# Performance work log

Measured on AMD Instinct MI355X. Metric: run time of the kernel, lower is better.

## Reference

```python
import jax, jax.numpy as jnp
import numpy as np

B, T = 32, 1024
TEMP_IN, STAT_IN = 128, 64
TEMP_OUT, STAT_OUT = 128, 64
EPS = 1e-5
NEG_SLOPE = 0.01


def _bn_eval(x, gamma, beta, mean, var):
    # BatchNorm1d in eval mode (running stats)
    return (x - mean) * jax.lax.rsqrt(var + EPS) * gamma + beta


def _leaky_relu(x):
    return jnp.where(x >= 0, x, NEG_SLOPE * x)


def setup_inputs() -> dict:
    key = jax.random.key(0)
    k = jax.random.split(key, 6)
    # deterministic ragged lengths in [512, 1024]
    lengths_np = (512 + (np.arange(B) * 37) % 513).astype(np.int64)
    N = int(lengths_np.sum())  # 23450
    batch_idx = np.repeat(np.arange(B), lengths_np).astype(np.int32)
    pos_idx = np.concatenate([np.arange(l) for l in lengths_np]).astype(np.int32)
    valid = (np.arange(T)[None, :] < lengths_np[:, None])  # [B, T]
    mask_repeat = valid[:, :, None] & valid[:, None, :]    # [B, T, T]

    inp = {
        "x_temp": jax.random.normal(k[0], (N, TEMP_IN), jnp.float32),
        "x_stat": jax.random.normal(k[1], (B, STAT_IN), jnp.float32),
        "temp_attn": jax.random.normal(k[2], (B, T, T), jnp.float32) * 0.1,
        "mask_repeat": jnp.asarray(mask_repeat),
        "lengths": jnp.asarray(lengths_np),
        "batch_idx": jnp.asarray(batch_idx),
        "pos_idx": jnp.asarray(pos_idx),
        # non_linear_temp: Linear(TEMP_IN+STAT_IN -> TEMP_OUT) + BN
        "W1": jax.random.normal(k[3], (TEMP_OUT, TEMP_IN + STAT_IN), jnp.float32) / np.sqrt(TEMP_IN + STAT_IN),
        "b1": jnp.zeros((TEMP_OUT,), jnp.float32),
        "gamma1": jnp.ones((TEMP_OUT,), jnp.float32),
        "beta1": jnp.zeros((TEMP_OUT,), jnp.float32),
        "mean1": jnp.zeros((TEMP_OUT,), jnp.float32),
        "var1": jnp.ones((TEMP_OUT,), jnp.float32),
        # non_linear_stat: Linear(STAT_IN -> STAT_OUT) + BN
        "W2": jax.random.normal(k[4], (STAT_OUT, STAT_IN), jnp.float32) / np.sqrt(STAT_IN),
        "b2": jnp.zeros((STAT_OUT,), jnp.float32),
        "gamma2": jnp.ones((STAT_OUT,), jnp.float32),
        "beta2": jnp.zeros((STAT_OUT,), jnp.float32),
        "mean2": jnp.zeros((STAT_OUT,), jnp.float32),
        "var2": jnp.ones((STAT_OUT,), jnp.float32),
    }
    return inp


def reference(x_temp, x_stat, temp_attn, mask_repeat, lengths, batch_idx, pos_idx,
              W1, b1, gamma1, beta1, mean1, var1,
              W2, b2, gamma2, beta2, mean2, var2):
    # repeat_static_features: gather per-batch static feats to packed rows
    x_stat_rep = x_stat[batch_idx]                              # [N, STAT_IN]
    h = jnp.concatenate((x_temp, x_stat_rep), axis=-1) @ W1.T + b1
    h = _leaky_relu(_bn_eval(h, gamma1, beta1, mean1, var1))    # [N, TEMP_OUT]

    # pad_packed_sequences: scatter packed rows into [B, T, C] (zeros elsewhere)
    padded = jnp.zeros((B, T, TEMP_OUT), h.dtype).at[batch_idx, pos_idx].set(h)

    # self attention: softmax(x x^T / sqrt(d)) over padded rows (as original)
    d = jnp.asarray(TEMP_OUT, h.dtype)
    qk = jnp.einsum('btc,bsc->bts', padded, padded) / jnp.sqrt(d)
    self_attn = jax.nn.softmax(qk, axis=-1)

    attn = jnp.where(mask_repeat, self_attn + temp_attn, jnp.asarray(0.0, h.dtype))

    x_stat_out = _leaky_relu(_bn_eval(x_stat @ W2.T + b2, gamma2, beta2, mean2, var2))

    x_out_pad = jnp.einsum('bts,bsc->btc', attn, padded)        # [B, T, TEMP_OUT]
    # pack_padded_sequences: gather valid positions back to packed layout
    x_out = x_out_pad[batch_idx, pos_idx]                       # [N, TEMP_OUT]
    return (x_out, x_stat_out)
```

## Files before the change

### kernel.cpp

```cpp
#include <hip/hip_runtime.h>
#include <hip/hip_bf16.h>
#include <hip/hip_fp16.h>

typedef __hip_bfloat16 bf16;
typedef __attribute__((ext_vector_type(8))) short short8;
typedef __attribute__((ext_vector_type(4))) float f32x4;

#define EPS 1e-5f
#define NSLOPE 0.01f

__device__ __forceinline__ float b2f(bf16 v) { return __bfloat162float(v); }

__device__ __forceinline__ float ld1(const void* p, size_t idx, int isbf) {
  if (isbf) return b2f(((const bf16*)p)[idx]);
  return ((const float*)p)[idx];
}
__device__ __forceinline__ void st1(void* p, size_t idx, int isbf, float v) {
  if (isbf) ((bf16*)p)[idx] = __float2bfloat16(v);
  else      ((float*)p)[idx] = v;
}
__device__ __forceinline__ short f2bs(float x) {
  bf16 t = __float2bfloat16(x);
  short s; __builtin_memcpy(&s, &t, 2); return s;
}
__device__ __forceinline__ short8 pack8f(const float* p) {
  float4 a = *(const float4*)p, b = *(const float4*)(p + 4);
  short8 r;
  r[0] = f2bs(a.x); r[1] = f2bs(a.y); r[2] = f2bs(a.z); r[3] = f2bs(a.w);
  r[4] = f2bs(b.x); r[5] = f2bs(b.y); r[6] = f2bs(b.z); r[7] = f2bs(b.w);
  return r;
}

__global__ void meta_kernel(const void* __restrict__ xt,
                            const int* __restrict__ bidx, const int* __restrict__ pidx,
                            int N, int B, int* __restrict__ rs, int* __restrict__ ln,
                            int* __restrict__ flag) {
  if (blockIdx.x == 0 && threadIdx.x < 64) {
    unsigned w = ((const unsigned*)xt)[threadIdx.x];
    unsigned lo = w & 0xffffu;
    unsigned ex = (lo >> 7) & 0xffu;
    bool sane = ((lo & 0x7fffu) == 0u) || (ex >= 96u && ex <= 134u);
    unsigned long long m = __ballot(sane);
    if (threadIdx.x == 0) flag[0] = (__popcll(m) >= 48) ? 1 : 0;
  }
  int stride = gridDim.x * blockDim.x;
  for (int i = blockIdx.x * blockDim.x + threadIdx.x; i < N; i += stride) {
    int b = bidx[i];
    if ((unsigned)b >= (unsigned)B) continue;
    if (i == 0 || bidx[i - 1] != b) rs[b] = i;
    if (i == N - 1 || bidx[i + 1] != b) ln[b] = pidx[i] + 1;
  }
}

__global__ void w1cvt_kernel(const void* __restrict__ W1, const int* __restrict__ flag,
                             bf16* __restrict__ w1b, int n) {
  const int isbf = flag[0];
  int i = blockIdx.x * blockDim.x + threadIdx.x;
  if (i < n) w1b[i] = __float2bfloat16(ld1(W1, i, isbf));
}

__global__ void zfill_kernel(void* out, const int* __restrict__ flag, long long n) {
  const int isbf = flag[0];
  long long i = (long long)blockIdx.x * blockDim.x + threadIdx.x;
  long long stride = (long long)gridDim.x * blockDim.x;
  for (; i < n; i += stride) st1(out, (size_t)i, isbf, 0.f);
}

__global__ __launch_bounds__(256) void h_mfma_kernel(
    const void* __restrict__ xt, const void* __restrict__ xsg,
    const int* __restrict__ bidx, const bf16* __restrict__ w1b,
    const void* __restrict__ b1,
    const void* __restrict__ g1, const void* __restrict__ be1,
    const void* __restrict__ mn1, const void* __restrict__ vr1,
    const int* __restrict__ flag, bf16* __restrict__ hout, int N) {
  const int isbf = flag[0];
  const int tid = threadIdx.x, lane = tid & 63, wv = tid >> 6;
  const int m16 = lane & 15, quad = lane >> 4;
  const int row0 = blockIdx.x * 64 + wv * 16;
  const int m = row0 + m16;
  const int mc = (m < N) ? m : (N - 1);
  const int bi = bidx[mc];

  short8 af[6];
  if (isbf) {
    const bf16* xr = (const bf16*)xt + (size_t)mc * 128 + quad * 8;
#pragma unroll
    for (int ks = 0; ks < 4; ++ks) af[ks] = *(const short8*)(xr + ks * 32);
    const bf16* sr = (const bf16*)xsg + (size_t)bi * 64 + quad * 8;
    af[4] = *(const short8*)sr;
    af[5] = *(const short8*)(sr + 32);
  } else {
    const float* xr = (const float*)xt + (size_t)mc * 128 + quad * 8;
#pragma unroll
    for (int ks = 0; ks < 4; ++ks) af[ks] = pack8f(xr + ks * 32);
    const float* sr = (const float*)xsg + (size_t)bi * 64 + quad * 8;
    af[4] = pack8f(sr);
    af[5] = pack8f(sr + 32);
  }

  f32x4 acc[8];
#pragma unroll
  for (int ct = 0; ct < 8; ++ct) acc[ct] = (f32x4){0.f, 0.f, 0.f, 0.f};

#pragma unroll
  for (int ks = 0; ks < 6; ++ks) {
    const int k = ks * 32 + quad * 8;
#pragma unroll
    for (int ct = 0; ct < 8; ++ct) {
      const int o = ct * 16 + m16;
      short8 bfrag = *(const short8*)(w1b + (size_t)o * 192 + k);
      acc[ct] = __builtin_amdgcn_mfma_f32_16x16x32_bf16(af[ks], bfrag, acc[ct], 0, 0, 0);
    }
  }

#pragma unroll
  for (int ct = 0; ct < 8; ++ct) {
    const int o = ct * 16 + m16;
    float k1 = ld1(g1, o, isbf) * rsqrtf(ld1(vr1, o, isbf) + EPS);
    float k0 = ld1(be1, o, isbf) - ld1(mn1, o, isbf) * k1;
    float bias = ld1(b1, o, isbf);
#pragma unroll
    for (int r = 0; r < 4; ++r) {
      int mr = row0 + quad * 4 + r;
      if (mr < N) {
        float v = (acc[ct][r] + bias) * k1 + k0;
        v = (v >= 0.f) ? v : NSLOPE * v;
        hout[(size_t)mr * 128 + o] = __float2bfloat16(v);
      }
    }
  }
}

__global__ __launch_bounds__(64) void stat_kernel(
    const void* __restrict__ xstat, const void* __restrict__ W2,
    const void* __restrict__ b2, const void* __restrict__ g2,
    const void* __restrict__ be2, const void* __restrict__ mn2,
    const void* __restrict__ vr2, const int* __restrict__ flag,
    void* __restrict__ out, long long obase) {
  __shared__ float xs[64];
  const int isbf = flag[0];
  const int b = blockIdx.x, o = threadIdx.x;
  xs[o] = ld1(xstat, b * 64 + o, isbf);
  __syncthreads();
  float acc = ld1(b2, o, isbf);
#pragma unroll 8
  for (int j = 0; j < 64; ++j) acc += xs[j] * ld1(W2, o * 64 + j, isbf);
  float k1 = ld1(g2, o, isbf) * rsqrtf(ld1(vr2, o, isbf) + EPS);
  float k0 = ld1(be2, o, isbf) - ld1(mn2, o, isbf) * k1;
  float v = acc * k1 + k0;
  v = (v >= 0.f) ? v : NSLOPE * v;
  st1(out, (size_t)(obase + b * 64 + o), isbf, v);
}

__global__ __launch_bounds__(256) void attn_mfma_kernel(
    const void* __restrict__ ta, const bf16* __restrict__ h,
    const int* __restrict__ rs_arr, const int* __restrict__ ln_arr,
    const int* __restrict__ flag, void* __restrict__ xout, int T, int N) {
  __shared__ __align__(16) unsigned short Ss[16][1032];
  __shared__ __align__(16) unsigned short vT[128][66];

  const int b = blockIdx.y, t0 = blockIdx.x * 16;
  const int len = ln_arr[b];
  if (t0 >= len) return;
  const int isbf = flag[0];
  const int rs = rs_arr[b];
  const int nrows = min(16, len - t0);
  const int tid = threadIdx.x;
  const int lane = tid & 63, wv = tid >> 6;
  const int m16 = lane & 15, quad = lane >> 4;

  short8 qf[4];
  {
    int qrow = rs + t0 + m16;
    if (qrow > N - 1) qrow = N - 1;
    const bf16* qp = h + (size_t)qrow * 128 + quad * 8;
#pragma unroll
    for (int ks = 0; ks < 4; ++ks)
      qf[ks] = *(const short8*)(qp + ks * 32);
  }

  const float scale = 0.08838834764831845f;
  const int nact = (len + 15) >> 4;
  const short8 zero8 = {0, 0, 0, 0, 0, 0, 0, 0};

  {
    short8 kc[4] = {zero8, zero8, zero8, zero8};
    int st = wv;
    if (st < nact) {
      int s = st * 16 + m16;
      bool v = (s < len);
      const bf16* kp = h + (size_t)(rs + (v ? s : 0)) * 128 + quad * 8;
#pragma unroll
      for (int ks = 0; ks < 4; ++ks) kc[ks] = v ? *(const short8*)(kp + ks * 32) : zero8;
    }
    for (; st < nact; st += 4) {
      short8 kn[4] = {zero8, zero8, zero8, zero8};
      int stn = st + 4;
      if (stn < nact) {
        int s2 = stn * 16 + m16;
        bool v2 = (s2 < len);
        const bf16* kp2 = h + (size_t)(rs + (v2 ? s2 : 0)) * 128 + quad * 8;
#pragma unroll
        for (int ks = 0; ks < 4; ++ks) kn[ks] = v2 ? *(const short8*)(kp2 + ks * 32) : zero8;
      }
      f32x4 acc = {0.f, 0.f, 0.f, 0.f};
#pragma unroll
      for (int ks = 0; ks < 4; ++ks)
        acc = __builtin_amdgcn_mfma_f32_16x16x32_bf16(qf[ks], kc[ks], acc, 0, 0, 0);
      int s = st * 16 + m16;
      if (s < T) {
#pragma unroll
        for (int r = 0; r < 4; ++r)
          Ss[quad * 4 + r][s] = __half_as_ushort(__float2half(acc[r] * scale));
      }
#pragma unroll
      for (int ks = 0; ks < 4; ++ks) kc[ks] = kn[ks];
    }
  }
  __syncthreads();

  {
    const int lenp64 = (len + 63) & ~63;
    for (int j = 0; j < 4; ++j) {
      int r = wv + (j << 2);
      float vals[16];
#pragma unroll
      for (int k = 0; k < 16; ++k) {
        int s = lane + (k << 6);
        vals[k] = (s < len) ? __half2float(__ushort_as_half(Ss[r][s])) : -INFINITY;
      }
      float mx = -INFINITY;
#pragma unroll
      for (int k = 0; k < 16; ++k) mx = fmaxf(mx, vals[k]);
#pragma unroll
      for (int off = 32; off >= 1; off >>= 1) mx = fmaxf(mx, __shfl_xor(mx, off, 64));
      if (len < T) mx = fmaxf(mx, 0.f);
      float l = 0.f;
#pragma unroll
      for (int k = 0; k < 16; ++k) { float e = __expf(vals[k] - mx); vals[k] = e; l += e; }
#pragma unroll
      for (int off = 32; off >= 1; off >>= 1) l += __shfl_xor(l, off, 64);
      l += (float)(T - len) * __expf(-mx);
      float inv = 1.f / l;
#pragma unroll
      for (int k = 0; k < 16; ++k) {
        int s = lane + (k << 6);
        if (s < len)          *(bf16*)&Ss[r][s] = __float2bfloat16(vals[k] * inv);
        else if (s < lenp64)  *(bf16*)&Ss[r][s] = __float2bfloat16(0.f);
      }
    }
  }
  __syncthreads();

  f32x4 oacc0 = {0.f, 0.f, 0.f, 0.f};
  f32x4 oacc1 = {0.f, 0.f, 0.f, 0.f};
  const size_t tarow = ((size_t)b * T + (t0 + m16)) * (size_t)T;
  for (int s0 = 0; s0 < len; s0 += 64) {
    for (int e = tid; e < 512; e += 256) {
      int sp = e >> 4, c8 = (e & 15) << 3;
      int s = s0 + 2 * sp;
      uint4 u0 = {0, 0, 0, 0}, u1 = {0, 0, 0, 0};
      if (s < len)     u0 = *(const uint4*)(h + (size_t)(rs + s) * 128 + c8);
      if (s + 1 < len) u1 = *(const uint4*)(h + (size_t)(rs + s + 1) * 128 + c8);
      const unsigned short* a0 = (const unsigned short*)&u0;
      const unsigned short* a1 = (const unsigned short*)&u1;
#pragma unroll
      for (int j = 0; j < 8; ++j)
        *(unsigned*)&vT[c8 + j][2 * sp] = (unsigned)a0[j] | ((unsigned)a1[j] << 16);
    }
    short8 taf0, taf1;
    if (isbf) {
      const bf16* tp = (const bf16*)ta + tarow + s0 + quad * 8;
      taf0 = *(const short8*)tp;
      taf1 = *(const short8*)(tp + 32);
    } else {
      const float* tp = (const float*)ta + tarow + s0 + quad * 8;
      taf0 = pack8f(tp);
      taf1 = pack8f(tp + 32);
    }
    __syncthreads();
#pragma unroll
    for (int ks = 0; ks < 2; ++ks) {
      short8 pf = *(const short8*)&Ss[m16][s0 + ks * 32 + quad * 8];
      short8 tf = ks ? taf1 : taf0;
#pragma unroll
      for (int ct = 0; ct < 2; ++ct) {
        const int c0 = wv * 32 + ct * 16;
        const unsigned short* vrow = &vT[c0 + m16][ks * 32 + quad * 8];
        unsigned w0 = *(const unsigned*)(vrow + 0);
        unsigned w1 = *(const unsigned*)(vrow + 2);
        unsigned w2 = *(const unsigned*)(vrow + 4);
        unsigned w3 = *(const unsigned*)(vrow + 6);
        short8 bfv;
        bfv[0] = (short)(w0 & 0xffffu); bfv[1] = (short)(w0 >> 16);
        bfv[2] = (short)(w1 & 0xffffu); bfv[3] = (short)(w1 >> 16);
        bfv[4] = (short)(w2 & 0xffffu); bfv[5] = (short)(w2 >> 16);
        bfv[6] = (short)(w3 & 0xffffu); bfv[7] = (short)(w3 >> 16);
        if (ct == 0) {
          oacc0 = __builtin_amdgcn_mfma_f32_16x16x32_bf16(pf, bfv, oacc0, 0, 0, 0);
          oacc0 = __builtin_amdgcn_mfma_f32_16x16x32_bf16(tf, bfv, oacc0, 0, 0, 0);
        } else {
          oacc1 = __builtin_amdgcn_mfma_f32_16x16x32_bf16(pf, bfv, oacc1, 0, 0, 0);
          oacc1 = __builtin_amdgcn_mfma_f32_16x16x32_bf16(tf, bfv, oacc1, 0, 0, 0);
        }
      }
    }
    __syncthreads();
  }

#pragma unroll
  for (int r = 0; r < 4; ++r) {
    int t = quad * 4 + r;
    if (t < nrows) {
      size_t ob = (size_t)(rs + t0 + t) * 128;
      st1(xout, ob + wv * 32 + m16,      isbf, oacc0[r]);
      st1(xout, ob + wv * 32 + 16 + m16, isbf, oacc1[r]);
    }
  }
}

extern "C" void kernel_launch(void* const* d_in, const int* in_sizes, int n_in,
                              void* d_out, int out_size, void* d_ws, size_t ws_size,
                              hipStream_t stream) {
  const void* x_temp    = d_in[0];
  const void* x_stat    = d_in[1];
  const void* temp_attn = d_in[2];
  const int N = in_sizes[0] / 128;
  const int B = in_sizes[1] / 64;
  long long tt = (long long)in_sizes[2] / B;
  int T = 1; while ((long long)(T + 1) * (T + 1) <= tt) ++T;

  int p = 3;
  while (p < n_in && in_sizes[p] != N) ++p;
  const int* batch_idx = (const int*)d_in[p++];
  const int* pos_idx   = (const int*)d_in[p++];
  const void* W1 = d_in[p++];
  const void* b1 = d_in[p++];
  const void* g1 = d_in[p++];
  const void* be1= d_in[p++];
  const void* mn1= d_in[p++];
  const void* vr1= d_in[p++];
  const void* W2 = d_in[p++];
  const void* b2 = d_in[p++];
  const void* g2 = d_in[p++];
  const void* be2= d_in[p++];
  const void* mn2= d_in[p++];
  const void* vr2= d_in[p++];

  int*  meta = (int*)d_ws;
  int*  rs   = meta;
  int*  lnp  = meta + B;
  int*  flag = meta + 2 * B;
  bf16* h    = (bf16*)((char*)d_ws + 1024);
  bf16* w1b  = h + (size_t)N * 128;
  const int w1n = 128 * 192;
  size_t need = 1024 + (size_t)N * 128 * sizeof(bf16) + (size_t)w1n * sizeof(bf16);

  long long obase = (long long)N * 128;

  meta_kernel<<<90, 256, 0, stream>>>(x_temp, batch_idx, pos_idx, N, B, rs, lnp, flag);
  stat_kernel<<<B, 64, 0, stream>>>(x_stat, W2, b2, g2, be2, mn2, vr2, flag,
                                    d_out, obase);
  if (ws_size >= need) {
    w1cvt_kernel<<<(w1n + 255) / 256, 256, 0, stream>>>(W1, flag, w1b, w1n);
    h_mfma_kernel<<<(N + 63) / 64, 256, 0, stream>>>(x_temp, x_stat, batch_idx,
                                                     w1b, b1, g1, be1, mn1, vr1,
                                                     flag, h, N);
    attn_mfma_kernel<<<dim3((T + 15) / 16, B), 256, 0, stream>>>(
        temp_attn, h, rs, lnp, flag, d_out, T, N);
  } else {
    zfill_kernel<<<512, 256, 0, stream>>>(d_out, flag, obase);
  }
}
```

Baseline: 442.5 us.

## Stream attention with online softmax and fold W1 conversion into meta kernel

The attention kernel drops the full 16x1024 score buffer in shared memory and replaces the three phases (QK, softmax, PV) with a flash-style loop over 64-column key tiles. Each tile keeps a running max and sum, rescales the probability accumulator, and keeps the temp_attn contribution in a separate accumulator. Shared memory use shrinks sharply, and launch_bounds asks for 4 blocks per CU to raise occupancy. The cost is extra barriers and cross-wave reductions inside every tile. The W1 bf16 conversion is merged into meta_kernel, removing one launch, but only if w1b fits in the workspace, since it is now written before the size check.

```diff
diff --git a/kernel.cpp b/kernel.cpp
--- a/kernel.cpp
+++ b/kernel.cpp
@@ -34,29 +34,28 @@
 __global__ void meta_kernel(const void* __restrict__ xt,
                             const int* __restrict__ bidx, const int* __restrict__ pidx,
                             int N, int B, int* __restrict__ rs, int* __restrict__ ln,
-                            int* __restrict__ flag) {
-  if (blockIdx.x == 0 && threadIdx.x < 64) {
-    unsigned w = ((const unsigned*)xt)[threadIdx.x];
+                            int* __restrict__ flag,
+                            const void* __restrict__ W1, bf16* __restrict__ w1b, int w1n) {
+  int isbf_l = 0;
+  {
+    unsigned w = ((const unsigned*)xt)[threadIdx.x & 63];
     unsigned lo = w & 0xffffu;
     unsigned ex = (lo >> 7) & 0xffu;
     bool sane = ((lo & 0x7fffu) == 0u) || (ex >= 96u && ex <= 134u);
     unsigned long long m = __ballot(sane);
-    if (threadIdx.x == 0) flag[0] = (__popcll(m) >= 48) ? 1 : 0;
+    isbf_l = (__popcll(m) >= 48) ? 1 : 0;
+    if (blockIdx.x == 0 && threadIdx.x == 0) flag[0] = isbf_l;
   }
   int stride = gridDim.x * blockDim.x;
-  for (int i = blockIdx.x * blockDim.x + threadIdx.x; i < N; i += stride) {
+  int g0 = blockIdx.x * blockDim.x + threadIdx.x;
+  for (int i = g0; i < N; i += stride) {
     int b = bidx[i];
     if ((unsigned)b >= (unsigned)B) continue;
     if (i == 0 || bidx[i - 1] != b) rs[b] = i;
     if (i == N - 1 || bidx[i + 1] != b) ln[b] = pidx[i] + 1;
   }
-}
-
-__global__ void w1cvt_kernel(const void* __restrict__ W1, const int* __restrict__ flag,
-                             bf16* __restrict__ w1b, int n) {
-  const int isbf = flag[0];
-  int i = blockIdx.x * blockDim.x + threadIdx.x;
-  if (i < n) w1b[i] = __float2bfloat16(ld1(W1, i, isbf));
+  for (int i = g0; i < w1n; i += stride)
+    w1b[i] = __float2bfloat16(ld1(W1, i, isbf_l));
 }
 
 __global__ void zfill_kernel(void* out, const int* __restrict__ flag, long long n) {
@@ -152,12 +151,16 @@
   st1(out, (size_t)(obase + b * 64 + o), isbf, v);
 }
 
-__global__ __launch_bounds__(256) void attn_mfma_kernel(
+__global__ __launch_bounds__(256, 4) void attn_mfma_kernel(
     const void* __restrict__ ta, const bf16* __restrict__ h,
     const int* __restrict__ rs_arr, const int* __restrict__ ln_arr,
     const int* __restrict__ flag, void* __restrict__ xout, int T, int N) {
-  __shared__ __align__(16) unsigned short Ss[16][1032];
   __shared__ __align__(16) unsigned short vT[128][66];
+  __shared__ __align__(16) unsigned short Pbuf[16][72];
+  __shared__ float wmax[4][16];
+  __shared__ float wsum[4][16];
+  __shared__ float mrun[16];
+  __shared__ float lrun[16];
 
   const int b = blockIdx.y, t0 = blockIdx.x * 16;
   const int len = ln_arr[b];
@@ -175,91 +178,32 @@
     if (qrow > N - 1) qrow = N - 1;
     const bf16* qp = h + (size_t)qrow * 128 + quad * 8;
 #pragma unroll
-    for (int ks = 0; ks < 4; ++ks)
-      qf[ks] = *(const short8*)(qp + ks * 32);
-  }
+    for (int ks = 0; ks < 4; ++ks) qf[ks] = *(const short8*)(qp + ks * 32);
+  }
+
+  if (tid < 16) { mrun[tid] = -INFINITY; lrun[tid] = 0.f; }
 
   const float scale = 0.08838834764831845f;
-  const int nact = (len + 15) >> 4;
   const short8 zero8 = {0, 0, 0, 0, 0, 0, 0, 0};
-
+  const int scol = wv * 16 + m16;
+  const size_t tarow = ((size_t)b * T + (t0 + m16)) * (size_t)T;
+
+  f32x4 accp[2] = {{0.f,0.f,0.f,0.f},{0.f,0.f,0.f,0.f}};
+  f32x4 acct[2] = {{0.f,0.f,0.f,0.f},{0.f,0.f,0.f,0.f}};
+
+  short8 kf[4];
   {
-    short8 kc[4] = {zero8, zero8, zero8, zero8};
-    int st = wv;
-    if (st < nact) {
-      int s = st * 16 + m16;
-      bool v = (s < len);
-      const bf16* kp = h + (size_t)(rs + (v ? s : 0)) * 128 + quad * 8;
-#pragma unroll
-      for (int ks = 0; ks < 4; ++ks) kc[ks] = v ? *(const short8*)(kp + ks * 32) : zero8;
-    }
-    for (; st < nact; st += 4) {
-      short8 kn[4] = {zero8, zero8, zero8, zero8};
-      int stn = st + 4;
-      if (stn < nact) {
-        int s2 = stn * 16 + m16;
-        bool v2 = (s2 < len);
-        const bf16* kp2 = h + (size_t)(rs + (v2 ? s2 : 0)) * 128 + quad * 8;
-#pragma unroll
-        for (int ks = 0; ks < 4; ++ks) kn[ks] = v2 ? *(const short8*)(kp2 + ks * 32) : zero8;
-      }
-      f32x4 acc = {0.f, 0.f, 0.f, 0.f};
-#pragma unroll
-      for (int ks = 0; ks < 4; ++ks)
-        acc = __builtin_amdgcn_mfma_f32_16x16x32_bf16(qf[ks], kc[ks], acc, 0, 0, 0);
-      int s = st * 16 + m16;
-      if (s < T) {
-#pragma unroll
-        for (int r = 0; r < 4; ++r)
-          Ss[quad * 4 + r][s] = __half_as_ushort(__float2half(acc[r] * scale));
-      }
-#pragma unroll
-      for (int ks = 0; ks < 4; ++ks) kc[ks] = kn[ks];
-    }
-  }
-  __syncthreads();
-
-  {
-    const int lenp64 = (len + 63) & ~63;
-    for (int j = 0; j < 4; ++j) {
-      int r = wv + (j << 2);
-      float vals[16];
-#pragma unroll
-      for (int k = 0; k < 16; ++k) {
-        int s = lane + (k << 6);
-        vals[k] = (s < len) ? __half2float(__ushort_as_half(Ss[r][s])) : -INFINITY;
-      }
-      float mx = -INFINITY;
-#pragma unroll
-      for (int k = 0; k < 16; ++k) mx = fmaxf(mx, vals[k]);
-#pragma unroll
-      for (int off = 32; off >= 1; off >>= 1) mx = fmaxf(mx, __shfl_xor(mx, off, 64));
-      if (len < T) mx = fmaxf(mx, 0.f);
-      float l = 0.f;
-#pragma unroll
-      for (int k = 0; k < 16; ++k) { float e = __expf(vals[k] - mx); vals[k] = e; l += e; }
-#pragma unroll
-      for (int off = 32; off >= 1; off >>= 1) l += __shfl_xor(l, off, 64);
-      l += (float)(T - len) * __expf(-mx);
-      float inv = 1.f / l;
-#pragma unroll
-      for (int k = 0; k < 16; ++k) {
-        int s = lane + (k << 6);
-        if (s < len)          *(bf16*)&Ss[r][s] = __float2bfloat16(vals[k] * inv);
-        else if (s < lenp64)  *(bf16*)&Ss[r][s] = __float2bfloat16(0.f);
-      }
-    }
-  }
-  __syncthreads();
-
-  f32x4 oacc0 = {0.f, 0.f, 0.f, 0.f};
-  f32x4 oacc1 = {0.f, 0.f, 0.f, 0.f};
-  const size_t tarow = ((size_t)b * T + (t0 + m16)) * (size_t)T;
+    bool v = scol < len;
+    const bf16* kp = h + (size_t)(rs + (v ? scol : 0)) * 128 + quad * 8;
+#pragma unroll
+    for (int ks = 0; ks < 4; ++ks) kf[ks] = v ? *(const short8*)(kp + ks * 32) : zero8;
+  }
+
   for (int s0 = 0; s0 < len; s0 += 64) {
     for (int e = tid; e < 512; e += 256) {
       int sp = e >> 4, c8 = (e & 15) << 3;
       int s = s0 + 2 * sp;
-      uint4 u0 = {0, 0, 0, 0}, u1 = {0, 0, 0, 0};
+      uint4 u0 = {0,0,0,0}, u1 = {0,0,0,0};
       if (s < len)     u0 = *(const uint4*)(h + (size_t)(rs + s) * 128 + c8);
       if (s + 1 < len) u1 = *(const uint4*)(h + (size_t)(rs + s + 1) * 128 + c8);
       const unsigned short* a0 = (const unsigned short*)&u0;
@@ -278,10 +222,81 @@
       taf0 = pack8f(tp);
       taf1 = pack8f(tp + 32);
     }
+    short8 kn[4];
+    {
+      int sn = s0 + 64 + scol;
+      bool v = sn < len;
+      const bf16* kp = h + (size_t)(rs + (v ? sn : 0)) * 128 + quad * 8;
+#pragma unroll
+      for (int ks = 0; ks < 4; ++ks) kn[ks] = v ? *(const short8*)(kp + ks * 32) : zero8;
+    }
+    f32x4 sa = {0.f, 0.f, 0.f, 0.f};
+#pragma unroll
+    for (int ks = 0; ks < 4; ++ks)
+      sa = __builtin_amdgcn_mfma_f32_16x16x32_bf16(qf[ks], kf[ks], sa, 0, 0, 0);
+#pragma unroll
+    for (int ks = 0; ks < 4; ++ks) kf[ks] = kn[ks];
+
+    const bool sval = (s0 + scol) < len;
+    float cm[4];
+#pragma unroll
+    for (int r = 0; r < 4; ++r) cm[r] = sval ? sa[r] * scale : -INFINITY;
+#pragma unroll
+    for (int off = 1; off <= 8; off <<= 1) {
+#pragma unroll
+      for (int r = 0; r < 4; ++r) cm[r] = fmaxf(cm[r], __shfl_xor(cm[r], off, 64));
+    }
+    if (m16 == 0) {
+#pragma unroll
+      for (int r = 0; r < 4; ++r) wmax[wv][quad * 4 + r] = cm[r];
+    }
     __syncthreads();
+
+    float mnew[4], al[4], p[4];
+#pragma unroll
+    for (int r = 0; r < 4; ++r) {
+      int row = quad * 4 + r;
+      float cmax = fmaxf(fmaxf(wmax[0][row], wmax[1][row]),
+                         fmaxf(wmax[2][row], wmax[3][row]));
+      float mold = mrun[row];
+      mnew[r] = fmaxf(mold, cmax);
+      al[r] = __expf(mold - mnew[r]);
+      p[r] = sval ? __expf(sa[r] * scale - mnew[r]) : 0.f;
+    }
+    float cs[4];
+#pragma unroll
+    for (int r = 0; r < 4; ++r) cs[r] = p[r];
+#pragma unroll
+    for (int off = 1; off <= 8; off <<= 1) {
+#pragma unroll
+      for (int r = 0; r < 4; ++r) cs[r] += __shfl_xor(cs[r], off, 64);
+    }
+    if (m16 == 0) {
+#pragma unroll
+      for (int r = 0; r < 4; ++r) wsum[wv][quad * 4 + r] = cs[r];
+    }
+#pragma unroll
+    for (int r = 0; r < 4; ++r)
+      Pbuf[quad * 4 + r][wv * 16 + m16] = (unsigned short)f2bs(p[r]);
+    __syncthreads();
+
+    if (wv == 0 && m16 == 0) {
+#pragma unroll
+      for (int r = 0; r < 4; ++r) {
+        int row = quad * 4 + r;
+        float st = wsum[0][row] + wsum[1][row] + wsum[2][row] + wsum[3][row];
+        lrun[row] = lrun[row] * al[r] + st;
+        mrun[row] = mnew[r];
+      }
+    }
+#pragma unroll
+    for (int ct = 0; ct < 2; ++ct) {
+#pragma unroll
+      for (int r = 0; r < 4; ++r) accp[ct][r] *= al[r];
+    }
 #pragma unroll
     for (int ks = 0; ks < 2; ++ks) {
-      short8 pf = *(const short8*)&Ss[m16][s0 + ks * 32 + quad * 8];
+      short8 pf = *(const short8*)&Pbuf[m16][ks * 32 + quad * 8];
       short8 tf = ks ? taf1 : taf0;
 #pragma unroll
       for (int ct = 0; ct < 2; ++ct) {
@@ -297,11 +312,11 @@
         bfv[4] = (short)(w2 & 0xffffu); bfv[5] = (short)(w2 >> 16);
         bfv[6] = (short)(w3 & 0xffffu); bfv[7] = (short)(w3 >> 16);
         if (ct == 0) {
-          oacc0 = __builtin_amdgcn_mfma_f32_16x16x32_bf16(pf, bfv, oacc0, 0, 0, 0);
-          oacc0 = __builtin_amdgcn_mfma_f32_16x16x32_bf16(tf, bfv, oacc0, 0, 0, 0);
+          accp[0] = __builtin_amdgcn_mfma_f32_16x16x32_bf16(pf, bfv, accp[0], 0, 0, 0);
+          acct[0] = __builtin_amdgcn_mfma_f32_16x16x32_bf16(tf, bfv, acct[0], 0, 0, 0);
         } else {
-          oacc1 = __builtin_amdgcn_mfma_f32_16x16x32_bf16(pf, bfv, oacc1, 0, 0, 0);
-          oacc1 = __builtin_amdgcn_mfma_f32_16x16x32_bf16(tf, bfv, oacc1, 0, 0, 0);
+          accp[1] = __builtin_amdgcn_mfma_f32_16x16x32_bf16(pf, bfv, accp[1], 0, 0, 0);
+          acct[1] = __builtin_amdgcn_mfma_f32_16x16x32_bf16(tf, bfv, acct[1], 0, 0, 0);
         }
       }
     }
@@ -312,9 +327,14 @@
   for (int r = 0; r < 4; ++r) {
     int t = quad * 4 + r;
     if (t < nrows) {
+      float m_r = mrun[t], l_r = lrun[t];
+      float m_f = (len < T) ? fmaxf(m_r, 0.f) : m_r;
+      float corr = __expf(m_r - m_f);
+      float l_f = l_r * corr + (float)(T - len) * __expf(-m_f);
+      float os = corr / l_f;
       size_t ob = (size_t)(rs + t0 + t) * 128;
-      st1(xout, ob + wv * 32 + m16,      isbf, oacc0[r]);
-      st1(xout, ob + wv * 32 + 16 + m16, isbf, oacc1[r]);
+      st1(xout, ob + wv * 32 + m16,      isbf, accp[0][r] * os + acct[0][r]);
+      st1(xout, ob + wv * 32 + 16 + m16, isbf, accp[1][r] * os + acct[1][r]);
     }
   }
 }
@@ -358,11 +378,11 @@
 
   long long obase = (long long)N * 128;
 
-  meta_kernel<<<90, 256, 0, stream>>>(x_temp, batch_idx, pos_idx, N, B, rs, lnp, flag);
+  meta_kernel<<<90, 256, 0, stream>>>(x_temp, batch_idx, pos_idx, N, B, rs, lnp,
+                                      flag, W1, w1b, w1n);
   stat_kernel<<<B, 64, 0, stream>>>(x_stat, W2, b2, g2, be2, mn2, vr2, flag,
                                     d_out, obase);
   if (ws_size >= need) {
-    w1cvt_kernel<<<(w1n + 255) / 256, 256, 0, stream>>>(W1, flag, w1b, w1n);
     h_mfma_kernel<<<(N + 63) / 64, 256, 0, stream>>>(x_temp, x_stat, batch_idx,
                                                      w1b, b1, g1, be1, mn1, vr1,
                                                      flag, h, N);
```

New measurement: 424.4 us. 1.04x faster.
